# Kernel optimization log

Hardware: AMD Instinct MI355X
Metric: run time of the kernel (lower is better)

The kernel has to match this reference:

```python
import jax, jax.numpy as jnp
import numpy as np

K = 5  # kernel_size per dim, dim=2 -> 25 kernel weights, degree-1 open B-splines


def _spline_basis(pseudo):
    """Degree-1 open B-spline basis for dim=2, kernel_size=5.
    pseudo: [E,2] in [0,1]. Returns basis [E,4], kernel index wi [E,4]."""
    v = pseudo * (K - 1)                      # [E,2]
    lo = jnp.floor(v)
    frac = v - lo                             # [E,2]
    lo = lo.astype(jnp.int32)
    b = jnp.stack([1.0 - frac, frac], axis=-1)            # [E,2,2] (edge, dim, offset)
    idx = jnp.clip(lo[..., None] + jnp.arange(2, dtype=jnp.int32), 0, K - 1)  # [E,2,2]
    basis = b[:, 0, :, None] * b[:, 1, None, :]           # [E,2,2]
    wi = idx[:, 0, :, None] + K * idx[:, 1, None, :]      # [E,2,2] (dim0 stride 1, dim1 stride K)
    E = pseudo.shape[0]
    return basis.reshape(E, 4), wi.reshape(E, 4)


def _spline_conv(x, src, dst, pseudo, W, root, bias, num_nodes):
    basis, wi = _spline_basis(pseudo)          # [E,4], [E,4]
    xW = jnp.einsum('ni,kio->nko', x, W)       # [N,25,out]
    gathered = xW[src[:, None], wi]            # [E,4,out]
    msg = jnp.einsum('es,eso->eo', basis, gathered)  # [E,out]
    agg = jax.ops.segment_max(msg, dst, num_segments=num_nodes)
    agg = jnp.where(jnp.isneginf(agg), 0.0, agg)  # empty segments -> 0 (PyG fill)
    return agg + x @ root + bias


def setup_inputs() -> dict:
    key = jax.random.key(0)
    ks = jax.random.split(key, 12)
    N, E, C = 50000, 800000, 64
    s = 1.0 / np.sqrt(C)
    return {
        'x': jax.random.normal(ks[0], (N, C), jnp.float32),
        'edge_index': jax.random.randint(ks[1], (2, E), 0, N, jnp.int32),
        'edge_attr': jax.random.uniform(ks[2], (E, 2), jnp.float32),
        'W1': jax.random.normal(ks[3], (25, C, C), jnp.float32) * s,
        'root1': jax.random.normal(ks[4], (C, C), jnp.float32) * s,
        'b1': jnp.zeros((C,), jnp.float32),
        'W2': jax.random.normal(ks[5], (25, C, C), jnp.float32) * s,
        'root2': jax.random.normal(ks[6], (C, C), jnp.float32) * s,
        'b2': jnp.zeros((C,), jnp.float32),
        'final_w': jax.random.normal(ks[7], (3 * C, C), jnp.float32) / np.sqrt(3 * C),
        'final_b': jnp.zeros((C,), jnp.float32),
    }


def reference(x, edge_index, edge_attr, W1, root1, b1, W2, root2, b2, final_w, final_b):
    N = x.shape[0]
    src, dst = edge_index[0], edge_index[1]
    x1 = jax.nn.relu(_spline_conv(x, src, dst, edge_attr, W1, root1, b1, N))
    x2 = jax.nn.relu(_spline_conv(x1, src, dst, edge_attr, W2, root2, b2, N))
    h = jnp.concatenate([x, x1, x2], axis=-1)   # cat=True; dropout p=0 (eval)
    return h @ final_w + final_b
```

## Files before the change

### kernel.cpp

```cpp
#include <hip/hip_runtime.h>
#include <hip/hip_bf16.h>


typedef short  bf16x8 __attribute__((ext_vector_type(8)));
typedef float  f32x4  __attribute__((ext_vector_type(4)));
typedef int    i32x4  __attribute__((ext_vector_type(4)));

__device__ __forceinline__ float bf2f(ushort u) {
    return __uint_as_float((uint)u << 16);
}
__device__ __forceinline__ ushort f2bf(float f) {
    uint u = __float_as_uint(f);
    return (ushort)((u + 0x7FFF + ((u >> 16) & 1)) >> 16);
}

__global__ __launch_bounds__(256) void prep(
    const float* __restrict__ x, ushort* __restrict__ xb, int nx,
    const float* __restrict__ W1, const float* __restrict__ r1, ushort* __restrict__ WtA,
    const float* __restrict__ W2, const float* __restrict__ r2, ushort* __restrict__ WtB,
    const float* __restrict__ fw, ushort* __restrict__ fwT,
    int* __restrict__ deg, int N)
{
    const int nw = 26 * 4096, nfw = 3 * 4096;
    int idx = blockIdx.x * 256 + threadIdx.x;
    if (idx < nx) { xb[idx] = f2bf(x[idx]); return; }
    idx -= nx;
    if (idx < nw) {
        int tile = idx >> 12, rem = idx & 4095, o = rem >> 6, i = rem & 63;
        WtA[idx] = f2bf(tile < 25 ? W1[tile * 4096 + i * 64 + o] : r1[i * 64 + o]);
        return;
    }
    idx -= nw;
    if (idx < nw) {
        int tile = idx >> 12, rem = idx & 4095, o = rem >> 6, i = rem & 63;
        WtB[idx] = f2bf(tile < 25 ? W2[tile * 4096 + i * 64 + o] : r2[i * 64 + o]);
        return;
    }
    idx -= nw;
    if (idx < nfw) {
        int t = idx >> 12, rem = idx & 4095, o = rem >> 6, k = rem & 63;
        fwT[idx] = f2bf(fw[(t * 64 + k) * 64 + o]);
        return;
    }
    idx -= nfw;
    if (idx < N) deg[idx] = 0;
}

__global__ __launch_bounds__(256) void hist_deg(
    const int* __restrict__ ei, int* __restrict__ deg, int E)
{
    int e = blockIdx.x * 256 + threadIdx.x;
    if (e < E) atomicAdd(&deg[ei[E + e]], 1);
}

__global__ __launch_bounds__(1024) void scan_block(
    const int* __restrict__ deg, int* __restrict__ inc,
    int* __restrict__ partial, int N)
{
    __shared__ int s[1024];
    int i = blockIdx.x * 1024 + threadIdx.x;
    int v = (i < N) ? deg[i] : 0;
    s[threadIdx.x] = v;
    __syncthreads();
    for (int off = 1; off < 1024; off <<= 1) {
        int t = (threadIdx.x >= off) ? s[threadIdx.x - off] : 0;
        __syncthreads();
        s[threadIdx.x] += t;
        __syncthreads();
    }
    if (i < N) inc[i] = s[threadIdx.x];
    if (threadIdx.x == 1023) partial[blockIdx.x] = s[1023];
}

__global__ void scan_partial(int* __restrict__ partial, int nb)
{
    __shared__ int s[64];
    int t = threadIdx.x;
    int v = (t < nb) ? partial[t] : 0;
    s[t] = v;
    __syncthreads();
    for (int off = 1; off < 64; off <<= 1) {
        int x = (t >= off) ? s[t - off] : 0;
        __syncthreads();
        s[t] += x;
        __syncthreads();
    }
    if (t < nb) partial[t] = s[t] - v;
}

__global__ __launch_bounds__(1024) void scan_finalize(
    const int* __restrict__ deg, const int* __restrict__ inc,
    const int* __restrict__ partial, int* __restrict__ row_ptr,
    int* __restrict__ cursor, int N)
{
    int i = blockIdx.x * 1024 + threadIdx.x;
    if (i >= N) return;
    int v = inc[i] + partial[blockIdx.x];
    row_ptr[i + 1] = v;
    cursor[i] = v - deg[i];
    if (i == 0) row_ptr[0] = 0;
}

__global__ __launch_bounds__(256) void gemm_scatter(
    const ushort* __restrict__ A, const ushort* __restrict__ Wt,
    ushort* __restrict__ xWb, ushort* __restrict__ xRoot, int mtiles,
    const int* __restrict__ ei, const float* __restrict__ attr,
    int* __restrict__ cursor, int4* __restrict__ epack, int E)
{
    __shared__ ushort Cs[4][16][72];
    const int bx = blockIdx.x;

    if (bx >= 26) {
        if (!ei) return;
        int e = ((bx - 26) * gridDim.y + blockIdx.y) * 256 + threadIdx.x;
        if (e >= E) return;
        int src = ei[e], dst = ei[E + e];
        float u = attr[2 * e] * 4.f;
        float v = attr[2 * e + 1] * 4.f;
        float lu = floorf(u), lv = floorf(v);
        float fu = u - lu, fv = v - lv;
        int iu = (int)lu;  iu = iu < 0 ? 0 : (iu > 4 ? 4 : iu);
        int iv = (int)lv;  iv = iv < 0 ? 0 : (iv > 4 ? 4 : iv);
        int iu1 = iu + 1 > 4 ? 4 : iu + 1;
        int iv1 = iv + 1 > 4 ? 4 : iv + 1;
        uint slots = (uint)(iu + 5 * iv) | ((uint)(iu + 5 * iv1) << 8) |
                     ((uint)(iu1 + 5 * iv) << 16) | ((uint)(iu1 + 5 * iv1) << 24);
        uint wlo = (uint)f2bf((1.f - fu) * (1.f - fv)) | ((uint)f2bf((1.f - fu) * fv) << 16);
        uint whi = (uint)f2bf(fu * (1.f - fv)) | ((uint)f2bf(fu * fv) << 16);
        int pos = atomicAdd(&cursor[dst], 1);
        i32x4 pk = {src * 3200, (int)slots, (int)wlo, (int)whi};
        __builtin_nontemporal_store(pk, (i32x4*)(epack + pos));
        return;
    }

    const int wave = threadIdx.x >> 6;
    const int lane = threadIdx.x & 63;
    const int l16 = lane & 15;
    const int half = lane >> 4;
    ushort (*cw)[72] = Cs[wave];

    const ushort* btile = Wt + (size_t)bx * 4096;
    bf16x8 b0[4], b1[4];
    #pragma unroll
    for (int s = 0; s < 4; ++s) {
        const ushort* brow = btile + (size_t)(s * 16 + l16) * 64;
        b0[s] = *(const bf16x8*)(brow + half * 8);
        b1[s] = *(const bf16x8*)(brow + 32 + half * 8);
    }

    const int mt_base = blockIdx.y * 8;
    const int nit = (mtiles - mt_base) < 8 ? (mtiles - mt_base) : 8;

    const ushort* arow0 = A + (size_t)(mt_base * 64 + wave * 16 + l16) * 64;
    bf16x8 a0 = *(const bf16x8*)(arow0 + half * 8);
    bf16x8 a1 = *(const bf16x8*)(arow0 + 32 + half * 8);

    for (int it = 0; it < nit; ++it) {
        const int m0 = (mt_base + it) * 64;
        const int m_base = m0 + wave * 16;

        bf16x8 na0, na1;
        if (it + 1 < nit) {
            const ushort* arow = A + (size_t)(m_base + 64 + l16) * 64;
            na0 = *(const bf16x8*)(arow + half * 8);
            na1 = *(const bf16x8*)(arow + 32 + half * 8);
        }

        f32x4 acc[4];
        #pragma unroll
        for (int s = 0; s < 4; ++s) {
            acc[s] = (f32x4){0.f, 0.f, 0.f, 0.f};
            acc[s] = __builtin_amdgcn_mfma_f32_16x16x32_bf16(a0, b0[s], acc[s], 0, 0, 0);
            acc[s] = __builtin_amdgcn_mfma_f32_16x16x32_bf16(a1, b1[s], acc[s], 0, 0, 0);
        }

        if (bx == 25) {
            #pragma unroll
            for (int s = 0; s < 4; ++s)
                #pragma unroll
                for (int r = 0; r < 4; ++r)
                    xRoot[(size_t)(m_base + half * 4 + r) * 64 + s * 16 + l16] = f2bf(acc[s][r]);
        } else {
            #pragma unroll
            for (int s = 0; s < 4; ++s)
                #pragma unroll
                for (int r = 0; r < 4; ++r)
                    cw[half * 4 + r][s * 16 + l16] = f2bf(acc[s][r]);
            #pragma unroll
            for (int i2 = 0; i2 < 2; ++i2) {
                int idx = i2 * 64 + lane;
                int row = idx >> 3, seg = idx & 7;
                uint4 v = *(const uint4*)&cw[row][seg * 8];
                *(uint4*)(xWb + (size_t)(m_base + row) * 1600 + bx * 64 + seg * 8) = v;
            }
        }
        a0 = na0; a1 = na1;
    }
}

__device__ __forceinline__ void gather4(
    const char* __restrict__ xwb, int lane, int rb, uint slots, ushort g[4])
{
    g[0] = *((const ushort*)(xwb + rb + ((slots & 255u) << 7)) + lane);
    g[1] = *((const ushort*)(xwb + rb + (((slots >> 8) & 255u) << 7)) + lane);
    g[2] = *((const ushort*)(xwb + rb + (((slots >> 16) & 255u) << 7)) + lane);
    g[3] = *((const ushort*)(xwb + rb + ((slots >> 24) << 7)) + lane);
}

__device__ __forceinline__ float consume4(const int4 d, const ushort g[4])
{
    float m = __uint_as_float((uint)d.z << 16) * bf2f(g[0]);
    m = fmaf(__uint_as_float((uint)d.z & 0xffff0000u), bf2f(g[1]), m);
    m = fmaf(__uint_as_float((uint)d.w << 16), bf2f(g[2]), m);
    m = fmaf(__uint_as_float((uint)d.w & 0xffff0000u), bf2f(g[3]), m);
    return m;
}

__global__ __launch_bounds__(256) void edge_csr(
    const ushort* __restrict__ xWb, const int* __restrict__ row_ptr,
    const int4* __restrict__ epack, const ushort* __restrict__ xRoot,
    const float* __restrict__ bias, float* __restrict__ outf,
    ushort* __restrict__ outb, int N)
{
    const int wv = __builtin_amdgcn_readfirstlane(threadIdx.x >> 6);
    const int d = blockIdx.x * 4 + wv;
    const int lane = threadIdx.x & 63;
    if (d >= N) return;
    const int e0 = __builtin_amdgcn_readfirstlane(row_ptr[d]);
    const int e1 = __builtin_amdgcn_readfirstlane(row_ptr[d + 1]);
    const char* xwb = (const char*)xWb;

    float vmax = -__builtin_inff();
    int e = e0;
    const int pairs = (e1 - e0) >> 1;
    if (pairs > 0) {
        int4 dA = epack[e], dB = epack[e + 1];
        ushort gA[4], gB[4];
        gather4(xwb, lane, dA.x, (uint)dA.y, gA);
        gather4(xwb, lane, dB.x, (uint)dB.y, gB);
        for (int p = 1; p < pairs; ++p) {
            int4 nA = epack[e + 2 * p], nB = epack[e + 2 * p + 1];
            ushort hA[4], hB[4];
            gather4(xwb, lane, nA.x, (uint)nA.y, hA);
            gather4(xwb, lane, nB.x, (uint)nB.y, hB);
            vmax = fmaxf(vmax, fmaxf(consume4(dA, gA), consume4(dB, gB)));
            #pragma unroll
            for (int i = 0; i < 4; ++i) { gA[i] = hA[i]; gB[i] = hB[i]; }
            dA = nA; dB = nB;
        }
        vmax = fmaxf(vmax, fmaxf(consume4(dA, gA), consume4(dB, gB)));
        e += pairs * 2;
    }
    if (e < e1) {
        int4 dA = epack[e];
        ushort gA[4];
        gather4(xwb, lane, dA.x, (uint)dA.y, gA);
        vmax = fmaxf(vmax, consume4(dA, gA));
    }
    if (e1 == e0) vmax = 0.f;
    float val = vmax + bf2f(xRoot[(size_t)d * 64 + lane]) + bias[lane];
    val = fmaxf(val, 0.f);
    if (outf) outf[(size_t)d * 64 + lane] = val;
    if (outb) outb[(size_t)d * 64 + lane] = f2bf(val);
}

__global__ __launch_bounds__(256) void final_mfma(
    const ushort* __restrict__ xb, const ushort* __restrict__ x1b,
    const ushort* __restrict__ x2b, const ushort* __restrict__ fwT,
    const float* __restrict__ fb, float* __restrict__ out, int M)
{
    const int wave = threadIdx.x >> 6;
    const int lane = threadIdx.x & 63;
    const int l16 = lane & 15;
    const int half = lane >> 4;
    const int m_base = blockIdx.x * 64 + wave * 16;
    const ushort* srcs[3] = {xb, x1b, x2b};

    f32x4 acc[4];
    #pragma unroll
    for (int s = 0; s < 4; ++s) acc[s] = (f32x4){0.f, 0.f, 0.f, 0.f};

    #pragma unroll
    for (int t = 0; t < 3; ++t) {
        const ushort* arow = srcs[t] + (size_t)(m_base + l16) * 64;
        bf16x8 a0 = *(const bf16x8*)(arow + half * 8);
        bf16x8 a1 = *(const bf16x8*)(arow + 32 + half * 8);
        const ushort* btile = fwT + (size_t)t * 4096;
        #pragma unroll
        for (int s = 0; s < 4; ++s) {
            const ushort* brow = btile + (size_t)(s * 16 + l16) * 64;
            bf16x8 b0 = *(const bf16x8*)(brow + half * 8);
            bf16x8 b1 = *(const bf16x8*)(brow + 32 + half * 8);
            acc[s] = __builtin_amdgcn_mfma_f32_16x16x32_bf16(a0, b0, acc[s], 0, 0, 0);
            acc[s] = __builtin_amdgcn_mfma_f32_16x16x32_bf16(a1, b1, acc[s], 0, 0, 0);
        }
    }

    #pragma unroll
    for (int s = 0; s < 4; ++s) {
        int o = s * 16 + l16;
        float b = fb[o];
        #pragma unroll
        for (int r = 0; r < 4; ++r) {
            int m = m_base + half * 4 + r;
            if (m < M) out[(size_t)m * 64 + o] = acc[s][r] + b;
        }
    }
}

extern "C" void kernel_launch(void* const* d_in, const int* in_sizes, int n_in,
                              void* d_out, int out_size, void* d_ws, size_t ws_size,
                              hipStream_t stream)
{
    const float* x    = (const float*)d_in[0];
    const int*   ei   = (const int*)d_in[1];
    const float* attr = (const float*)d_in[2];
    const float* W1   = (const float*)d_in[3];
    const float* r1   = (const float*)d_in[4];
    const float* b1   = (const float*)d_in[5];
    const float* W2   = (const float*)d_in[6];
    const float* r2   = (const float*)d_in[7];
    const float* b2   = (const float*)d_in[8];
    const float* fw   = (const float*)d_in[9];
    const float* fb   = (const float*)d_in[10];
    float* out = (float*)d_out;

    const int N = in_sizes[0] / 64;
    const int E = in_sizes[1] / 2;
    const int mtiles = (N + 63) / 64;
    const int Npad = mtiles * 64;

    char* p = (char*)d_ws;
    auto alloc = [&](size_t bytes) { void* q = p; p += (bytes + 255) & ~(size_t)255; return q; };
    int4*   epack  = (int4*)alloc((size_t)E * 16);
    ushort* xRoot  = (ushort*)alloc((size_t)Npad * 64 * 2);
    ushort* xWb    = (ushort*)alloc((size_t)Npad * 1600 * 2);
    ushort* xb     = (ushort*)alloc((size_t)Npad * 64 * 2);
    ushort* x1b    = (ushort*)alloc((size_t)Npad * 64 * 2);
    ushort* x2b    = (ushort*)alloc((size_t)Npad * 64 * 2);
    ushort* WtA    = (ushort*)alloc((size_t)26 * 4096 * 2);
    ushort* WtB    = (ushort*)alloc((size_t)26 * 4096 * 2);
    ushort* fwT    = (ushort*)alloc((size_t)3 * 4096 * 2);
    int*    deg    = (int*)alloc((size_t)N * 4);
    int*    cursor = (int*)alloc((size_t)N * 4);
    int*    rowp   = (int*)alloc((size_t)(N + 1) * 4);
    int*    tmpinc = (int*)alloc((size_t)N * 4);
    int*    part   = (int*)alloc(64 * 4);

    const int nb = (N + 1023) / 1024;

    const int nprep = N * 64 + 2 * 26 * 4096 + 3 * 4096 + N;
    prep<<<(nprep + 255) / 256, 256, 0, stream>>>(
        x, xb, N * 64, W1, r1, WtA, W2, r2, WtB, fw, fwT, deg, N);

    hist_deg<<<(E + 255) / 256, 256, 0, stream>>>(ei, deg, E);
    scan_block<<<nb, 1024, 0, stream>>>(deg, tmpinc, part, N);
    scan_partial<<<1, 64, 0, stream>>>(part, nb);
    scan_finalize<<<nb, 1024, 0, stream>>>(deg, tmpinc, part, rowp, cursor, N);

    const int gy = (mtiles + 7) / 8;
    const int sc_blocks = (E + 255) / 256;
    const int sc_cols = (sc_blocks + gy - 1) / gy;

    gemm_scatter<<<dim3(26 + sc_cols, gy), 256, 0, stream>>>(
        xb, WtA, xWb, xRoot, mtiles, ei, attr, cursor, epack, E);
    edge_csr<<<(N + 3) / 4, 256, 0, stream>>>(xWb, rowp, epack, xRoot, b1, nullptr, x1b, N);

    gemm_scatter<<<dim3(26, gy), 256, 0, stream>>>(
        x1b, WtB, xWb, xRoot, mtiles, nullptr, nullptr, nullptr, nullptr, E);
    edge_csr<<<(N + 3) / 4, 256, 0, stream>>>(xWb, rowp, epack, xRoot, b2, nullptr, x2b, N);

    final_mfma<<<mtiles, 256, 0, stream>>>(xb, x1b, x2b, fwT, fb, out, N);
}
```

Baseline: 385.7 us.

## Compute spline messages per edge via bucketed MFMA instead of dense xW table

Replaces the dense per-node precompute of x·W for all 25 kernel weights with a per-edge computation. Edges are bucketed by spline cell so each 64-edge tile shares the same four weight matrices. Each tile gathers source features, runs MFMA against those four matrices, weights the results by the basis values and writes one message per edge in CSR order. A simple segment-max pass then reduces the messages. This avoids writing and randomly gathering a 50000x1600 bf16 table. The cost is redundant per-edge GEMM work, extra bucketing and scatter kernels, and an E×64 message buffer.

Result: slower. 476.4 us (+23.5%).

```diff
diff --git a/kernel.cpp b/kernel.cpp
--- a/kernel.cpp
+++ b/kernel.cpp
@@ -19,7 +19,7 @@
     const float* __restrict__ W1, const float* __restrict__ r1, ushort* __restrict__ WtA,
     const float* __restrict__ W2, const float* __restrict__ r2, ushort* __restrict__ WtB,
     const float* __restrict__ fw, ushort* __restrict__ fwT,
-    int* __restrict__ deg, int N)
+    int* __restrict__ dstat, int Nz)
 {
     const int nw = 26 * 4096, nfw = 3 * 4096;
     int idx = blockIdx.x * 256 + threadIdx.x;
@@ -43,14 +43,28 @@
         return;
     }
     idx -= nfw;
-    if (idx < N) deg[idx] = 0;
+    if (idx < Nz) dstat[idx] = 0;
 }
 
 __global__ __launch_bounds__(256) void hist_deg(
-    const int* __restrict__ ei, int* __restrict__ deg, int E)
-{
-    int e = blockIdx.x * 256 + threadIdx.x;
-    if (e < E) atomicAdd(&deg[ei[E + e]], 1);
+    const int* __restrict__ ei, const float* __restrict__ attr,
+    int* __restrict__ deg, int* __restrict__ bcount, int E)
+{
+    __shared__ int lb[25];
+    int t = threadIdx.x;
+    if (t < 25) lb[t] = 0;
+    __syncthreads();
+    int e = blockIdx.x * 256 + t;
+    if (e < E) {
+        atomicAdd(&deg[ei[E + e]], 1);
+        float u = attr[2 * e] * 4.f;
+        float v = attr[2 * e + 1] * 4.f;
+        int iu = (int)floorf(u);  iu = iu < 0 ? 0 : (iu > 4 ? 4 : iu);
+        int iv = (int)floorf(v);  iv = iv < 0 ? 0 : (iv > 4 ? 4 : iv);
+        atomicAdd(&lb[iu + 5 * iv], 1);
+    }
+    __syncthreads();
+    if (t < 25 && lb[t] > 0) atomicAdd(&bcount[t], lb[t]);
 }
 
 __global__ __launch_bounds__(1024) void scan_block(
@@ -101,45 +115,73 @@
     if (i == 0) row_ptr[0] = 0;
 }
 
-__global__ __launch_bounds__(256) void gemm_scatter(
-    const ushort* __restrict__ A, const ushort* __restrict__ Wt,
-    ushort* __restrict__ xWb, ushort* __restrict__ xRoot, int mtiles,
+__global__ void bucket_setup(const int* __restrict__ bcount,
+                             int* __restrict__ boff, uint4* __restrict__ recs, int E)
+{
+    __shared__ int sb[26], sc[25];
+    int t = threadIdx.x;
+    if (t == 0) {
+        int acc = 0;
+        for (int b = 0; b < 25; ++b) {
+            sb[b] = acc; boff[b] = acc; sc[b] = bcount[b];
+            acc += (bcount[b] + 63) & ~63;
+        }
+        sb[25] = acc; boff[25] = acc;
+    }
+    __syncthreads();
+    uint4 z = make_uint4(0u, 0u, 0u, (uint)E);
+    for (int b = 0; b < 25; ++b) {
+        int start = sb[b] + sc[b], end = sb[b + 1];
+        for (int i = start + t; i < end; i += 64) recs[i] = z;
+    }
+}
+
+__global__ __launch_bounds__(256) void scatter_recs(
     const int* __restrict__ ei, const float* __restrict__ attr,
-    int* __restrict__ cursor, int4* __restrict__ epack, int E)
-{
-    __shared__ ushort Cs[4][16][72];
-    const int bx = blockIdx.x;
-
-    if (bx >= 26) {
-        if (!ei) return;
-        int e = ((bx - 26) * gridDim.y + blockIdx.y) * 256 + threadIdx.x;
-        if (e >= E) return;
-        int src = ei[e], dst = ei[E + e];
+    int* __restrict__ cursor, int* __restrict__ bcur,
+    const int* __restrict__ boff, uint4* __restrict__ recs, int E)
+{
+    __shared__ int lcnt[25], lbase[25];
+    int t = threadIdx.x;
+    if (t < 25) lcnt[t] = 0;
+    __syncthreads();
+    int e = blockIdx.x * 256 + t;
+    bool act = e < E;
+    int b = 0, rank = 0, src = 0, dst = 0;
+    float fu = 0.f, fv = 0.f;
+    if (act) {
+        src = ei[e]; dst = ei[E + e];
         float u = attr[2 * e] * 4.f;
         float v = attr[2 * e + 1] * 4.f;
         float lu = floorf(u), lv = floorf(v);
-        float fu = u - lu, fv = v - lv;
+        fu = u - lu; fv = v - lv;
         int iu = (int)lu;  iu = iu < 0 ? 0 : (iu > 4 ? 4 : iu);
         int iv = (int)lv;  iv = iv < 0 ? 0 : (iv > 4 ? 4 : iv);
-        int iu1 = iu + 1 > 4 ? 4 : iu + 1;
-        int iv1 = iv + 1 > 4 ? 4 : iv + 1;
-        uint slots = (uint)(iu + 5 * iv) | ((uint)(iu + 5 * iv1) << 8) |
-                     ((uint)(iu1 + 5 * iv) << 16) | ((uint)(iu1 + 5 * iv1) << 24);
+        b = iu + 5 * iv;
+        rank = atomicAdd(&lcnt[b], 1);
+    }
+    __syncthreads();
+    if (t < 25 && lcnt[t] > 0) lbase[t] = atomicAdd(&bcur[t], lcnt[t]);
+    __syncthreads();
+    if (act) {
         uint wlo = (uint)f2bf((1.f - fu) * (1.f - fv)) | ((uint)f2bf((1.f - fu) * fv) << 16);
         uint whi = (uint)f2bf(fu * (1.f - fv)) | ((uint)f2bf(fu * fv) << 16);
         int pos = atomicAdd(&cursor[dst], 1);
-        i32x4 pk = {src * 3200, (int)slots, (int)wlo, (int)whi};
-        __builtin_nontemporal_store(pk, (i32x4*)(epack + pos));
-        return;
-    }
-
+        int rpos = boff[b] + lbase[b] + rank;
+        i32x4 pk = {src * 128, (int)wlo, (int)whi, pos};
+        __builtin_nontemporal_store(pk, (i32x4*)(recs + rpos));
+    }
+}
+
+__global__ __launch_bounds__(256) void root_gemm(
+    const ushort* __restrict__ A, const ushort* __restrict__ Wt,
+    ushort* __restrict__ xRoot, int mtiles)
+{
     const int wave = threadIdx.x >> 6;
     const int lane = threadIdx.x & 63;
     const int l16 = lane & 15;
     const int half = lane >> 4;
-    ushort (*cw)[72] = Cs[wave];
-
-    const ushort* btile = Wt + (size_t)bx * 4096;
+    const ushort* btile = Wt + (size_t)25 * 4096;
     bf16x8 b0[4], b1[4];
     #pragma unroll
     for (int s = 0; s < 4; ++s) {
@@ -147,25 +189,13 @@
         b0[s] = *(const bf16x8*)(brow + half * 8);
         b1[s] = *(const bf16x8*)(brow + 32 + half * 8);
     }
-
-    const int mt_base = blockIdx.y * 8;
+    const int mt_base = blockIdx.x * 8;
     const int nit = (mtiles - mt_base) < 8 ? (mtiles - mt_base) : 8;
-
-    const ushort* arow0 = A + (size_t)(mt_base * 64 + wave * 16 + l16) * 64;
-    bf16x8 a0 = *(const bf16x8*)(arow0 + half * 8);
-    bf16x8 a1 = *(const bf16x8*)(arow0 + 32 + half * 8);
-
     for (int it = 0; it < nit; ++it) {
-        const int m0 = (mt_base + it) * 64;
-        const int m_base = m0 + wave * 16;
-
-        bf16x8 na0, na1;
-        if (it + 1 < nit) {
-            const ushort* arow = A + (size_t)(m_base + 64 + l16) * 64;
-            na0 = *(const bf16x8*)(arow + half * 8);
-            na1 = *(const bf16x8*)(arow + 32 + half * 8);
-        }
-
+        const int m_base = (mt_base + it) * 64 + wave * 16;
+        const ushort* arow = A + (size_t)(m_base + l16) * 64;
+        bf16x8 a0 = *(const bf16x8*)(arow + half * 8);
+        bf16x8 a1 = *(const bf16x8*)(arow + 32 + half * 8);
         f32x4 acc[4];
         #pragma unroll
         for (int s = 0; s < 4; ++s) {
@@ -173,53 +203,114 @@
             acc[s] = __builtin_amdgcn_mfma_f32_16x16x32_bf16(a0, b0[s], acc[s], 0, 0, 0);
             acc[s] = __builtin_amdgcn_mfma_f32_16x16x32_bf16(a1, b1[s], acc[s], 0, 0, 0);
         }
-
-        if (bx == 25) {
+        #pragma unroll
+        for (int s = 0; s < 4; ++s)
             #pragma unroll
-            for (int s = 0; s < 4; ++s)
-                #pragma unroll
-                for (int r = 0; r < 4; ++r)
-                    xRoot[(size_t)(m_base + half * 4 + r) * 64 + s * 16 + l16] = f2bf(acc[s][r]);
-        } else {
+            for (int r = 0; r < 4; ++r)
+                xRoot[(size_t)(m_base + half * 4 + r) * 64 + s * 16 + l16] = f2bf(acc[s][r]);
+    }
+}
+
+struct ShA {
+    int    srcS[64];
+    int    posS[64];
+    float4 wS[64];
+    ushort xg[16][72];
+    ushort cs[16][72];
+};
+
+__global__ __launch_bounds__(256) void spline_mm(
+    const ushort* __restrict__ X, const ushort* __restrict__ Wt,
+    const uint4* __restrict__ recs, const int* __restrict__ boff,
+    ushort* __restrict__ msg)
+{
+    __shared__ ShA sh[4];
+    const int wave = threadIdx.x >> 6;
+    const int lane = threadIdx.x & 63;
+    const int tile = blockIdx.x * 4 + wave;
+    const int t64 = tile * 64;
+    if (t64 >= boff[25]) return;
+    ShA& S = sh[wave];
+
+    int b = 0;
+    #pragma unroll
+    for (int i = 1; i < 25; ++i) b += (t64 >= boff[i]) ? 1 : 0;
+    const int iu = b % 5, iv = b / 5;
+    const int iu1 = (iu + 1 > 4) ? 4 : iu + 1;
+    const int iv1 = (iv + 1 > 4) ? 4 : iv + 1;
+    const int slot[4] = {iu + 5 * iv, iu + 5 * iv1, iu1 + 5 * iv, iu1 + 5 * iv1};
+
+    {
+        uint4 r = recs[t64 + lane];
+        S.srcS[lane] = (int)r.x;
+        S.posS[lane] = (int)r.w;
+        S.wS[lane] = make_float4(bf2f((ushort)(r.y & 0xffff)), bf2f((ushort)(r.y >> 16)),
+                                 bf2f((ushort)(r.z & 0xffff)), bf2f((ushort)(r.z >> 16)));
+    }
+
+    const int l16 = lane & 15, half = lane >> 4;
+    const int rr = lane >> 2, q = lane & 3;
+    const char* xp = (const char*)X;
+
+    for (int rt = 0; rt < 4; ++rt) {
+        {
+            int so = S.srcS[rt * 16 + rr];
+            uint4 v0 = *(const uint4*)(xp + so + q * 16);
+            uint4 v1 = *(const uint4*)(xp + so + q * 16 + 64);
+            *(uint4*)&S.xg[rr][q * 8] = v0;
+            *(uint4*)&S.xg[rr][q * 8 + 32] = v1;
+        }
+        bf16x8 a0 = *(const bf16x8*)&S.xg[l16][half * 8];
+        bf16x8 a1 = *(const bf16x8*)&S.xg[l16][32 + half * 8];
+        float4 w4[4];
+        #pragma unroll
+        for (int r = 0; r < 4; ++r) w4[r] = S.wS[rt * 16 + half * 4 + r];
+
+        f32x4 macc[4];
+        #pragma unroll
+        for (int s = 0; s < 4; ++s) macc[s] = (f32x4){0.f, 0.f, 0.f, 0.f};
+
+        #pragma unroll
+        for (int sl = 0; sl < 4; ++sl) {
+            const ushort* btile = Wt + (size_t)slot[sl] * 4096;
             #pragma unroll
-            for (int s = 0; s < 4; ++s)
-                #pragma unroll
-                for (int r = 0; r < 4; ++r)
-                    cw[half * 4 + r][s * 16 + l16] = f2bf(acc[s][r]);
+            for (int s = 0; s < 4; ++s) {
+                const ushort* brow = btile + (size_t)(s * 16 + l16) * 64;
+                bf16x8 b0 = *(const bf16x8*)(brow + half * 8);
+                bf16x8 b1 = *(const bf16x8*)(brow + 32 + half * 8);
+                f32x4 c = (f32x4){0.f, 0.f, 0.f, 0.f};
+                c = __builtin_amdgcn_mfma_f32_16x16x32_bf16(a0, b0, c, 0, 0, 0);
+                c = __builtin_amdgcn_mfma_f32_16x16x32_bf16(a1, b1, c, 0, 0, 0);
+                const float ws0 = (sl == 0) ? w4[0].x : (sl == 1) ? w4[0].y : (sl == 2) ? w4[0].z : w4[0].w;
+                const float ws1 = (sl == 0) ? w4[1].x : (sl == 1) ? w4[1].y : (sl == 2) ? w4[1].z : w4[1].w;
+                const float ws2 = (sl == 0) ? w4[2].x : (sl == 1) ? w4[2].y : (sl == 2) ? w4[2].z : w4[2].w;
+                const float ws3 = (sl == 0) ? w4[3].x : (sl == 1) ? w4[3].y : (sl == 2) ? w4[3].z : w4[3].w;
+                macc[s][0] = fmaf(ws0, c[0], macc[s][0]);
+                macc[s][1] = fmaf(ws1, c[1], macc[s][1]);
+                macc[s][2] = fmaf(ws2, c[2], macc[s][2]);
+                macc[s][3] = fmaf(ws3, c[3], macc[s][3]);
+            }
+        }
+
+        #pragma unroll
+        for (int s = 0; s < 4; ++s)
             #pragma unroll
-            for (int i2 = 0; i2 < 2; ++i2) {
-                int idx = i2 * 64 + lane;
-                int row = idx >> 3, seg = idx & 7;
-                uint4 v = *(const uint4*)&cw[row][seg * 8];
-                *(uint4*)(xWb + (size_t)(m_base + row) * 1600 + bx * 64 + seg * 8) = v;
-            }
-        }
-        a0 = na0; a1 = na1;
-    }
-}
-
-__device__ __forceinline__ void gather4(
-    const char* __restrict__ xwb, int lane, int rb, uint slots, ushort g[4])
-{
-    g[0] = *((const ushort*)(xwb + rb + ((slots & 255u) << 7)) + lane);
-    g[1] = *((const ushort*)(xwb + rb + (((slots >> 8) & 255u) << 7)) + lane);
-    g[2] = *((const ushort*)(xwb + rb + (((slots >> 16) & 255u) << 7)) + lane);
-    g[3] = *((const ushort*)(xwb + rb + ((slots >> 24) << 7)) + lane);
-}
-
-__device__ __forceinline__ float consume4(const int4 d, const ushort g[4])
-{
-    float m = __uint_as_float((uint)d.z << 16) * bf2f(g[0]);
-    m = fmaf(__uint_as_float((uint)d.z & 0xffff0000u), bf2f(g[1]), m);
-    m = fmaf(__uint_as_float((uint)d.w << 16), bf2f(g[2]), m);
-    m = fmaf(__uint_as_float((uint)d.w & 0xffff0000u), bf2f(g[3]), m);
-    return m;
-}
-
-__global__ __launch_bounds__(256) void edge_csr(
-    const ushort* __restrict__ xWb, const int* __restrict__ row_ptr,
-    const int4* __restrict__ epack, const ushort* __restrict__ xRoot,
-    const float* __restrict__ bias, float* __restrict__ outf,
+            for (int r = 0; r < 4; ++r)
+                S.cs[half * 4 + r][s * 16 + l16] = f2bf(macc[s][r]);
+        #pragma unroll
+        for (int i2 = 0; i2 < 2; ++i2) {
+            int idx = i2 * 64 + lane;
+            int row = idx >> 3, seg = idx & 7;
+            i32x4 v = *(const i32x4*)&S.cs[row][seg * 8];
+            int pos = S.posS[rt * 16 + row];
+            __builtin_nontemporal_store(v, (i32x4*)(msg + (size_t)pos * 64 + seg * 8));
+        }
+    }
+}
+
+__global__ __launch_bounds__(256) void edge_max(
+    const ushort* __restrict__ msg, const int* __restrict__ row_ptr,
+    const ushort* __restrict__ xRoot, const float* __restrict__ bias,
     ushort* __restrict__ outb, int N)
 {
     const int wv = __builtin_amdgcn_readfirstlane(threadIdx.x >> 6);
@@ -228,40 +319,23 @@
     if (d >= N) return;
     const int e0 = __builtin_amdgcn_readfirstlane(row_ptr[d]);
     const int e1 = __builtin_amdgcn_readfirstlane(row_ptr[d + 1]);
-    const char* xwb = (const char*)xWb;
+    const int cnt = e1 - e0;
+    const ushort* mp = msg + (size_t)e0 * 64 + lane;
 
     float vmax = -__builtin_inff();
-    int e = e0;
-    const int pairs = (e1 - e0) >> 1;
-    if (pairs > 0) {
-        int4 dA = epack[e], dB = epack[e + 1];
-        ushort gA[4], gB[4];
-        gather4(xwb, lane, dA.x, (uint)dA.y, gA);
-        gather4(xwb, lane, dB.x, (uint)dB.y, gB);
-        for (int p = 1; p < pairs; ++p) {
-            int4 nA = epack[e + 2 * p], nB = epack[e + 2 * p + 1];
-            ushort hA[4], hB[4];
-            gather4(xwb, lane, nA.x, (uint)nA.y, hA);
-            gather4(xwb, lane, nB.x, (uint)nB.y, hB);
-            vmax = fmaxf(vmax, fmaxf(consume4(dA, gA), consume4(dB, gB)));
-            #pragma unroll
-            for (int i = 0; i < 4; ++i) { gA[i] = hA[i]; gB[i] = hB[i]; }
-            dA = nA; dB = nB;
-        }
-        vmax = fmaxf(vmax, fmaxf(consume4(dA, gA), consume4(dB, gB)));
-        e += pairs * 2;
-    }
-    if (e < e1) {
-        int4 dA = epack[e];
-        ushort gA[4];
-        gather4(xwb, lane, dA.x, (uint)dA.y, gA);
-        vmax = fmaxf(vmax, consume4(dA, gA));
-    }
-    if (e1 == e0) vmax = 0.f;
+    int i = 0;
+    for (; i + 4 <= cnt; i += 4) {
+        float m0 = bf2f(mp[(size_t)(i + 0) * 64]);
+        float m1 = bf2f(mp[(size_t)(i + 1) * 64]);
+        float m2 = bf2f(mp[(size_t)(i + 2) * 64]);
+        float m3 = bf2f(mp[(size_t)(i + 3) * 64]);
+        vmax = fmaxf(vmax, fmaxf(fmaxf(m0, m1), fmaxf(m2, m3)));
+    }
+    for (; i < cnt; ++i) vmax = fmaxf(vmax, bf2f(mp[(size_t)i * 64]));
+    if (cnt == 0) vmax = 0.f;
     float val = vmax + bf2f(xRoot[(size_t)d * 64 + lane]) + bias[lane];
     val = fmaxf(val, 0.f);
-    if (outf) outf[(size_t)d * 64 + lane] = val;
-    if (outb) outb[(size_t)d * 64 + lane] = f2bf(val);
+    outb[(size_t)d * 64 + lane] = f2bf(val);
 }
 
 __global__ __launch_bounds__(256) void final_mfma(
@@ -332,43 +406,52 @@
 
     char* p = (char*)d_ws;
     auto alloc = [&](size_t bytes) { void* q = p; p += (bytes + 255) & ~(size_t)255; return q; };
-    int4*   epack  = (int4*)alloc((size_t)E * 16);
+    uint4*  recs   = (uint4*)alloc((size_t)(E + 1600) * 16);
+    ushort* msg    = (ushort*)alloc((size_t)(E + 1) * 64 * 2);
     ushort* xRoot  = (ushort*)alloc((size_t)Npad * 64 * 2);
-    ushort* xWb    = (ushort*)alloc((size_t)Npad * 1600 * 2);
     ushort* xb     = (ushort*)alloc((size_t)Npad * 64 * 2);
     ushort* x1b    = (ushort*)alloc((size_t)Npad * 64 * 2);
     ushort* x2b    = (ushort*)alloc((size_t)Npad * 64 * 2);
     ushort* WtA    = (ushort*)alloc((size_t)26 * 4096 * 2);
     ushort* WtB    = (ushort*)alloc((size_t)26 * 4096 * 2);
     ushort* fwT    = (ushort*)alloc((size_t)3 * 4096 * 2);
-    int*    deg    = (int*)alloc((size_t)N * 4);
+    int*    dstat  = (int*)alloc((size_t)(N + 64) * 4);
     int*    cursor = (int*)alloc((size_t)N * 4);
     int*    rowp   = (int*)alloc((size_t)(N + 1) * 4);
     int*    tmpinc = (int*)alloc((size_t)N * 4);
     int*    part   = (int*)alloc(64 * 4);
+    int*    boff   = (int*)alloc(32 * 4);
+
+    int* deg    = dstat;
+    int* bcount = dstat + N;
+    int* bcur   = dstat + N + 25;
 
     const int nb = (N + 1023) / 1024;
 
-    const int nprep = N * 64 + 2 * 26 * 4096 + 3 * 4096 + N;
+    const int Nz = N + 50;
+    const int nprep = N * 64 + 2 * 26 * 4096 + 3 * 4096 + Nz;
     prep<<<(nprep + 255) / 256, 256, 0, stream>>>(
-        x, xb, N * 64, W1, r1, WtA, W2, r2, WtB, fw, fwT, deg, N);
-
-    hist_deg<<<(E + 255) / 256, 256, 0, stream>>>(ei, deg, E);
+        x, xb, N * 64, W1, r1, WtA, W2, r2, WtB, fw, fwT, dstat, Nz);
+
+    hist_deg<<<(E + 255) / 256, 256, 0, stream>>>(ei, attr, deg, bcount, E);
     scan_block<<<nb, 1024, 0, stream>>>(deg, tmpinc, part, N);
     scan_partial<<<1, 64, 0, stream>>>(part, nb);
     scan_finalize<<<nb, 1024, 0, stream>>>(deg, tmpinc, part, rowp, cursor, N);
+    bucket_setup<<<1, 64, 0, stream>>>(bcount, boff, recs, E);
+
+    scatter_recs<<<(E + 255) / 256, 256, 0, stream>>>(
+        ei, attr, cursor, bcur, boff, recs, E);
 
     const int gy = (mtiles + 7) / 8;
-    const int sc_blocks = (E + 255) / 256;
-    const int sc_cols = (sc_blocks + gy - 1) / gy;
-
-    gemm_scatter<<<dim3(26 + sc_cols, gy), 256, 0, stream>>>(
-        xb, WtA, xWb, xRoot, mtiles, ei, attr, cursor, epack, E);
-    edge_csr<<<(N + 3) / 4, 256, 0, stream>>>(xWb, rowp, epack, xRoot, b1, nullptr, x1b, N);
-
-    gemm_scatter<<<dim3(26, gy), 256, 0, stream>>>(
-        x1b, WtB, xWb, xRoot, mtiles, nullptr, nullptr, nullptr, nullptr, E);
-    edge_csr<<<(N + 3) / 4, 256, 0, stream>>>(xWb, rowp, epack, xRoot, b2, nullptr, x2b, N);
+    const int nblkA = (E + 1600 + 255) / 256;
+
+    root_gemm<<<gy, 256, 0, stream>>>(xb, WtA, xRoot, mtiles);
+    spline_mm<<<nblkA, 256, 0, stream>>>(xb, WtA, recs, boff, msg);
+    edge_max<<<(N + 3) / 4, 256, 0, stream>>>(msg, rowp, xRoot, b1, x1b, N);
+
+    root_gemm<<<gy, 256, 0, stream>>>(x1b, WtB, xRoot, mtiles);
+    spline_mm<<<nblkA, 256, 0, stream>>>(x1b, WtB, recs, boff, msg);
+    edge_max<<<(N + 3) / 4, 256, 0, stream>>>(msg, rowp, xRoot, b2, x2b, N);
 
     final_mfma<<<mtiles, 256, 0, stream>>>(xb, x1b, x2b, fwT, fb, out, N);
 }
```
